# Optimization experiments

Hardware: AMD Instinct MI355X
Metric: run time of the kernel (lower is better)

Reference implementation:

```python
import jax, jax.numpy as jnp
import numpy as np
from jax import lax

INIT_STRIDE = 10.0
COARSE_STRIDE = 4.0
DOWN_SAMPLE = 4.0
NUM_POINT = 128
N_INST = 2000


def setup_inputs() -> dict:
    key = jax.random.key(0)
    ks = jax.random.split(key, 12)
    B, C, H, W = 4, 64, 256, 256
    return {
        'cnn_feature': jax.random.normal(ks[0], (B, C, H, W), jnp.float32),
        'wh_pred': jax.random.normal(ks[1], (B, NUM_POINT * 2, H, W), jnp.float32),
        'ct_ind': jax.random.randint(ks[2], (N_INST,), 0, H * W, jnp.int64 if jax.config.jax_enable_x64 else jnp.int32),
        'ct_img_idx': jax.random.randint(ks[3], (N_INST,), 0, B, jnp.int64 if jax.config.jax_enable_x64 else jnp.int32),
        'conv1_w': jax.random.normal(ks[4], (256, 64, 3, 3), jnp.float32) * 0.05,
        'conv1_b': jax.random.normal(ks[5], (256,), jnp.float32) * 0.05,
        'conv2_w': jax.random.normal(ks[6], (64, 256, 1, 1), jnp.float32) * 0.05,
        'conv2_b': jax.random.normal(ks[7], (64,), jnp.float32) * 0.05,
        'w_poly': jax.random.normal(ks[8], (NUM_POINT * 4, (NUM_POINT + 1) * 64), jnp.float32) * 0.02,
        'w_fuse': jax.random.normal(ks[9], (NUM_POINT * 2, NUM_POINT * 4), jnp.float32) * 0.02,
        'b_fuse': jax.random.normal(ks[10], (NUM_POINT * 2,), jnp.float32) * 0.02,
    }


def bilinear_sample(feat, pts, img_idx):
    # feat [B,C,H,W]; pts [N,P,2] pixel coords; img_idx [N]
    # matches torch grid_sample(align_corners=False, padding_mode='zeros')
    # with grid = pts/(WH/2) - 1  =>  sample coord = pts - 0.5
    B, C, H, W = feat.shape
    sx = pts[..., 0] - 0.5
    sy = pts[..., 1] - 0.5
    x0 = jnp.floor(sx).astype(jnp.int32); x1 = x0 + 1
    y0 = jnp.floor(sy).astype(jnp.int32); y1 = y0 + 1
    wx1 = sx - x0; wx0 = 1.0 - wx1
    wy1 = sy - y0; wy0 = 1.0 - wy1
    bidx = img_idx[:, None].astype(jnp.int32)  # [N,1]

    def corner(yc, xc, w):
        valid = (xc >= 0) & (xc < W) & (yc >= 0) & (yc < H)
        g = feat[bidx, :, jnp.clip(yc, 0, H - 1), jnp.clip(xc, 0, W - 1)]  # [N,P,C]
        return g * (w * valid)[..., None]

    out = (corner(y0, x0, wy0 * wx0) + corner(y0, x1, wy0 * wx1)
           + corner(y1, x0, wy1 * wx0) + corner(y1, x1, wy1 * wx1))
    return out  # [N,P,C]


def _forward(cnn_feature, wh_pred, ct_ind, ct_img_idx, conv1_w, conv1_b, conv2_w, conv2_b, w_poly, w_fuse, b_fuse):
    B, Cf, H, W = cnn_feature.shape
    N = ct_ind.shape[0]
    ct_x = jnp.clip(ct_ind % W, 0, W - 1)
    ct_y = jnp.clip(ct_ind // W, 0, H - 1)
    # gather polygon offsets at center locations: [N, 2*P] -> [N, P, 2]
    ct_offset = wh_pred[ct_img_idx, :, ct_y, ct_x].reshape(N, NUM_POINT, 2)
    ct = jnp.stack([ct_x, ct_y], axis=1).astype(jnp.float32)  # [N,2]
    init_polys = ct_offset * INIT_STRIDE + ct[:, None, :]  # [N,P,2]

    # Refine.trans_feature: conv3x3(64->256)+ReLU -> conv1x1(256->64)
    dn = ('NCHW', 'OIHW', 'NCHW')
    f = lax.conv_general_dilated(cnn_feature, conv1_w, (1, 1), 'SAME', dimension_numbers=dn) + conv1_b[None, :, None, None]
    f = jax.nn.relu(f)
    f = lax.conv_general_dilated(f, conv2_w, (1, 1), 'VALID', dimension_numbers=dn) + conv2_b[None, :, None, None]

    points = jnp.concatenate([ct[:, None, :], init_polys], axis=1)  # [N,P+1,2]
    fp = bilinear_sample(f, points, ct_img_idx)  # [N,P+1,64]
    fp = fp.transpose(0, 2, 1).reshape(N, -1)  # [N, 64*(P+1)] (C-major like torch)

    off = fp @ w_poly.T            # trans_poly (no bias)
    off = off @ w_fuse.T + b_fuse  # trans_fuse
    off = off.reshape(N, NUM_POINT, 2)
    coarse_polys = off * COARSE_STRIDE + lax.stop_gradient(init_polys)
    # stacked outputs: poly_init*down, poly_coarse*down -> [2,N,P,2]
    return jnp.stack([init_polys * DOWN_SAMPLE, coarse_polys * DOWN_SAMPLE])


def reference(cnn_feature, wh_pred, ct_ind, ct_img_idx, conv1_w, conv1_b, conv2_w, conv2_b, w_poly, w_fuse, b_fuse):
    return _forward(cnn_feature, wh_pred, ct_ind, ct_img_idx, conv1_w, conv1_b, conv2_w, conv2_b, w_poly, w_fuse, b_fuse)
```

## Files before the change

kernel.cpp:

```cpp
#include <hip/hip_runtime.h>

typedef unsigned short ushort_t;
typedef __bf16 bf16x8 __attribute__((ext_vector_type(8)));
typedef float f32x4 __attribute__((ext_vector_type(4)));

__device__ __forceinline__ ushort_t f2b(float f) {
  union { float f; unsigned u; } v; v.f = f;
  unsigned r = v.u + 0x7FFFu + ((v.u >> 16) & 1u);
  return (ushort_t)(r >> 16);
}
__device__ __forceinline__ float b2f(ushort_t u) {
  union { unsigned u; float f; } v; v.u = ((unsigned)u) << 16;
  return v.f;
}
__device__ __forceinline__ f32x4 MFMA(bf16x8 a, bf16x8 b, f32x4 c) {
  return __builtin_amdgcn_mfma_f32_16x16x32_bf16(a, b, c, 0, 0, 0);
}
__device__ __forceinline__ void gload_lds16(const ushort_t* g, ushort_t* l) {
  __builtin_amdgcn_global_load_lds(
      (const __attribute__((address_space(1))) unsigned int*)g,
      (__attribute__((address_space(3))) unsigned int*)l, 16, 0, 0);
}

#define XTW 258

__global__ void zero_border_kernel(ushort_t* __restrict__ xt) {
  int i = blockIdx.x * 256 + threadIdx.x;
  if (i >= 32896) return;
  int px_id = i >> 3, oct = (i & 7) << 3;
  int img = px_id / 1028, r = px_id - img * 1028;
  int row, col;
  if (r < 516) { row = (r < 258) ? 0 : 257; col = (r < 258) ? r : r - 258; }
  else { int rr = r - 516; row = 1 + (rr >> 1); col = (rr & 1) ? 257 : 0; }
  uint4 z = make_uint4(0, 0, 0, 0);
  *(uint4*)(xt + (((size_t)img * XTW + row) * XTW + col) * 64 + oct) = z;
}

__global__ void cast_xt_kernel(const float* __restrict__ x, ushort_t* __restrict__ xt) {
  __shared__ float tile[64][65];
  int blk = blockIdx.x;
  int b = blk >> 10, rest = blk & 1023;
  int y = rest >> 2, xseg = (rest & 3) << 6;
  int p0 = y * 256 + xseg;
  int t = threadIdx.x;
#pragma unroll
  for (int rep = 0; rep < 16; ++rep) {
    int lin = rep * 256 + t;
    int c = lin >> 6, p = lin & 63;
    tile[c][p] = x[((size_t)(b * 64 + c)) * 65536 + p0 + p];
  }
  __syncthreads();
#pragma unroll
  for (int rep = 0; rep < 2; ++rep) {
    int u = rep * 256 + t;
    int p = u >> 3, cc = (u & 7) << 3;
    union { ushort_t s[8]; uint4 v; } pk;
#pragma unroll
    for (int j = 0; j < 8; ++j) pk.s[j] = f2b(tile[cc + j][p]);
    int gx = xseg + p + 1;
    size_t base = (((size_t)b * XTW + (y + 1)) * XTW + gx) * 64;
    *(uint4*)(xt + base + (cc ^ ((gx & 7) << 3))) = pk.v;
  }
}

__global__ void cast_w1t_kernel(const float* __restrict__ w1, ushort_t* __restrict__ w1t) {
  int i = blockIdx.x * 256 + threadIdx.x;
  int tap = i >> 14;
  int rem = i & 16383;
  int nn = rem >> 6, c = rem & 63;
  int cs = c ^ ((nn & 7) << 3);
  w1t[tap * 16384 + nn * 64 + cs] = f2b(w1[(nn * 64 + c) * 9 + tap]);
}

__global__ void cast_f32_bf16_kernel(const float* __restrict__ src, ushort_t* __restrict__ dst, int n) {
  for (int i = blockIdx.x * blockDim.x + threadIdx.x; i < n; i += gridDim.x * blockDim.x)
    dst[i] = f2b(src[i]);
}

__global__ void prep_kernel(const float* __restrict__ wh, const int* __restrict__ ct_ind,
                            const int* __restrict__ ct_b, float* __restrict__ out,
                            float* __restrict__ pts) {
  int n = blockIdx.x, t = threadIdx.x;
  int ci = ct_ind[n];
  int b = ct_b[n];
  int ctx = ci & 255;
  int cty = (ci >> 8) & 255;
  float fx = (float)ctx, fy = (float)cty;
  size_t base = ((size_t)b * 256 + 2 * t) * 65536 + (size_t)cty * 256 + ctx;
  float ox = wh[base];
  float oy = wh[base + 65536];
  float ix = ox * 10.f + fx, iy = oy * 10.f + fy;
  out[(n * 128 + t) * 2]     = ix * 4.f;
  out[(n * 128 + t) * 2 + 1] = iy * 4.f;
  float* pn = pts + (size_t)n * 258;
  if (t == 0) { pn[0] = fx; pn[1] = fy; }
  pn[2 + t * 2] = ix;
  pn[3 + t * 2] = iy;
}

__global__ __launch_bounds__(512, 1)
void conv_fused_kernel(const ushort_t* __restrict__ xt, const ushort_t* __restrict__ w1t,
                       const float* __restrict__ b1, const float* __restrict__ w2,
                       const float* __restrict__ b2, ushort_t* __restrict__ f2) {
  __shared__ __align__(16) char smem[163840];
  ushort_t* strip = (ushort_t*)smem;
  ushort_t* Bb0   = (ushort_t*)(smem + 69632);
  ushort_t* Bb1   = (ushort_t*)(smem + 102400);
  ushort_t* F1    = (ushort_t*)smem;
  ushort_t* W2l   = (ushort_t*)(smem + 131072);
  ushort_t* T     = (ushort_t*)smem;

  int rawblk = blockIdx.x;
  int blk = ((rawblk & 7) << 7) + (rawblk >> 3);
  int b = blk >> 8;
  int rest = blk & 255;
  int y2 = (rest >> 1) << 1;
  int x0 = (rest & 1) << 7;
  int tid = threadIdx.x;
  int wid = tid >> 6, lane = tid & 63;
  int l15 = lane & 15, lg = lane >> 4;
  int wm = (wid >> 1) << 6;
  int wn = (wid & 1) << 7;

#pragma unroll
  for (int j = 0; j < 4; ++j) {
    int q = (wid << 2) + j;
    gload_lds16(w1t + q * 512 + lane * 8, Bb0 + q * 512);
  }
#pragma unroll
  for (int j = 0; j < 4; ++j) {
    int q = (wid << 2) + j;
    gload_lds16(w1t + 16384 + q * 512 + lane * 8, Bb1 + q * 512);
  }
  for (int c = wid; c < 68; c += 8) {
    int ry = c / 17, ck = c - ry * 17;
    const ushort_t* g = xt + (((size_t)b * XTW + (y2 + ry)) * XTW + x0 + ck * 8) * 64 + lane * 8;
    gload_lds16(g, strip + (ry * 136 + ck * 8) * 64);
  }
  asm volatile("s_waitcnt vmcnt(0) lgkmcnt(0)" ::: "memory");
  asm volatile("s_barrier" ::: "memory");

  f32x4 acc[4][8] = {};

#pragma unroll
  for (int tap = 0; tap < 9; ++tap) {
    const int dy = tap / 3 - 1, dx = tap % 3 - 1;
    ushort_t* Bcur = (tap & 1) ? Bb1 : Bb0;
    if (tap < 8) {
      ushort_t* Bnxt = (tap & 1) ? Bb0 : Bb1;
      const ushort_t* gb = w1t + (tap + 1) * 16384;
#pragma unroll
      for (int j = 0; j < 4; ++j) {
        int q = (wid << 2) + j;
        gload_lds16(gb + q * 512 + lane * 8, Bnxt + q * 512);
      }
    }
    const int sr  = (wm >> 7) + dy + 1;
    const int spb = (wm & 127) + dx + 1;
#pragma unroll
    for (int kk = 0; kk < 2; ++kk) {
      int c0 = (kk << 5) + (lg << 3);
      bf16x8 a[4];
#pragma unroll
      for (int m = 0; m < 4; ++m) {
        int sp = spb + m * 16 + l15;
        a[m] = *(const bf16x8*)(strip + ((sr * 136 + sp) << 6) + (c0 ^ ((sp & 7) << 3)));
      }
#pragma unroll
      for (int nf = 0; nf < 8; ++nf) {
        int br = wn + nf * 16 + l15;
        bf16x8 bb = *(const bf16x8*)(Bcur + (br << 6) + (c0 ^ ((br & 7) << 3)));
#pragma unroll
        for (int m = 0; m < 4; ++m)
          acc[m][nf] = MFMA(a[m], bb, acc[m][nf]);
      }
    }
    if (tap < 8) {
      asm volatile("s_waitcnt vmcnt(0)" ::: "memory");
      asm volatile("s_barrier" ::: "memory");
    }
  }
  __syncthreads();

#pragma unroll
  for (int nf = 0; nf < 8; ++nf) {
    int ch = wn + nf * 16 + l15;
    float bias = b1[ch];
#pragma unroll
    for (int m = 0; m < 4; ++m) {
#pragma unroll
      for (int r = 0; r < 4; ++r) {
        int p = wm + m * 16 + lg * 4 + r;
        F1[(p << 8) + (ch ^ ((p & 7) << 3))] = f2b(fmaxf(acc[m][nf][r] + bias, 0.f));
      }
    }
  }
#pragma unroll
  for (int it = 0; it < 4; ++it) {
    int u = it * 512 + tid;
    int oc = u >> 5, ic = (u & 31) << 3;
    float4 fa = *(const float4*)(w2 + (oc << 8) + ic);
    float4 fb = *(const float4*)(w2 + (oc << 8) + ic + 4);
    union { ushort_t s[8]; uint4 v; } pk;
    pk.s[0] = f2b(fa.x); pk.s[1] = f2b(fa.y); pk.s[2] = f2b(fa.z); pk.s[3] = f2b(fa.w);
    pk.s[4] = f2b(fb.x); pk.s[5] = f2b(fb.y); pk.s[6] = f2b(fb.z); pk.s[7] = f2b(fb.w);
    *(uint4*)(W2l + (oc << 8) + (ic ^ ((oc & 7) << 3))) = pk.v;
  }
  __syncthreads();
  int wpx = wid << 5;
  f32x4 acc2[2][4] = {};
#pragma unroll
  for (int kc = 0; kc < 8; ++kc) {
    int c0 = (kc << 5) + (lg << 3);
    bf16x8 a2[2];
#pragma unroll
    for (int mm = 0; mm < 2; ++mm) {
      int p = wpx + mm * 16 + l15;
      a2[mm] = *(const bf16x8*)(F1 + (p << 8) + (c0 ^ ((p & 7) << 3)));
    }
#pragma unroll
    for (int nf = 0; nf < 4; ++nf) {
      int oc = nf * 16 + l15;
      bf16x8 bw = *(const bf16x8*)(W2l + (oc << 8) + (c0 ^ ((oc & 7) << 3)));
#pragma unroll
      for (int mm = 0; mm < 2; ++mm)
        acc2[mm][nf] = MFMA(a2[mm], bw, acc2[mm][nf]);
    }
  }
  __syncthreads();
#pragma unroll
  for (int mm = 0; mm < 2; ++mm)
#pragma unroll
    for (int nf = 0; nf < 4; ++nf) {
      int oc = nf * 16 + l15;
      float bias = b2[oc];
#pragma unroll
      for (int r = 0; r < 4; ++r) {
        int p = wpx + mm * 16 + lg * 4 + r;
        T[(p << 6) + (oc ^ ((p & 7) << 3))] = f2b(acc2[mm][nf][r] + bias);
      }
    }
  __syncthreads();
  const size_t imgbase = (size_t)b * 65536;
#pragma unroll
  for (int it = 0; it < 4; ++it) {
    int u = it * 512 + tid;
    int p = u >> 3, co = (u & 7) << 3;
    uint4 v = *(const uint4*)(T + (p << 6) + (co ^ ((p & 7) << 3)));
    int gpx = (y2 + (p >> 7)) * 256 + x0 + (p & 127);
    *(uint4*)(f2 + (imgbase + gpx) * 64 + co) = v;
  }
}

__global__ void sample_kernel(const ushort_t* __restrict__ f2, const float* __restrict__ pts,
                              const int* __restrict__ ct_b, ushort_t* __restrict__ fp) {
  int n = blockIdx.x, t = threadIdx.x;
  __shared__ float pl[258];
  __shared__ __align__(16) ushort_t fpl[8256];
  int b = ct_b[n];
  const ushort_t* fb = f2 + (size_t)b * 4194304;
  for (int i = t; i < 258; i += 128) pl[i] = pts[(size_t)n * 258 + i];
  __syncthreads();
  int c4 = t & 15;
  int ps = t >> 4;
  for (int base = 0; base < 136; base += 8) {
    int pt = base + ps;
    bool live = pt < 129;
    int ptc = live ? pt : 0;
    float px = pl[ptc * 2], py = pl[ptc * 2 + 1];
    float sx = px - 0.5f, sy = py - 0.5f;
    float fx0 = floorf(sx), fy0 = floorf(sy);
    int x0 = (int)fx0, y0 = (int)fy0;
    float wx1 = sx - fx0, wy1 = sy - fy0;
    float wx0 = 1.f - wx1, wy0 = 1.f - wy1;
    float a0 = 0.f, a1 = 0.f, a2 = 0.f, a3 = 0.f;
#pragma unroll
    for (int cy = 0; cy < 2; ++cy) {
#pragma unroll
      for (int cx = 0; cx < 2; ++cx) {
        int yc = y0 + cy, xc = x0 + cx;
        float w = (cy ? wy1 : wy0) * (cx ? wx1 : wx0);
        bool valid = (xc >= 0) && (xc < 256) && (yc >= 0) && (yc < 256);
        int ycc = min(max(yc, 0), 255), xcc = min(max(xc, 0), 255);
        uint2 v = *(const uint2*)(fb + ((size_t)(ycc * 256 + xcc)) * 64 + (c4 << 2));
        float ww = valid ? w : 0.f;
        a0 += b2f((ushort_t)(v.x & 0xFFFF)) * ww;
        a1 += b2f((ushort_t)(v.x >> 16)) * ww;
        a2 += b2f((ushort_t)(v.y & 0xFFFF)) * ww;
        a3 += b2f((ushort_t)(v.y >> 16)) * ww;
      }
    }
    if (live) {
      int ch = c4 << 2;
      fpl[(ch + 0) * 129 + pt] = f2b(a0);
      fpl[(ch + 1) * 129 + pt] = f2b(a1);
      fpl[(ch + 2) * 129 + pt] = f2b(a2);
      fpl[(ch + 3) * 129 + pt] = f2b(a3);
    }
  }
  __syncthreads();
  uint4* fo = (uint4*)(fp + (size_t)n * 8256);
  const uint4* fi = (const uint4*)fpl;
  for (int i = t; i < 1032; i += 128) fo[i] = fi[i];
}

__global__ __launch_bounds__(256)
void gemm_splitk_kernel(const ushort_t* __restrict__ A, const ushort_t* __restrict__ B,
                        float* __restrict__ partials) {
  __shared__ ushort_t Alds[64][72];
  __shared__ ushort_t Blds[64][72];
  int spatial = blockIdx.x;
  int kc = blockIdx.y;
  int xcd = spatial & 7, j = spatial >> 3;
  int m_t = (xcd << 2) + (j >> 3);
  int n_t = j & 7;
  int m0 = m_t << 6, n0 = n_t << 6;
  int ks0 = (129 * kc) >> 3, ks1 = (129 * (kc + 1)) >> 3;

  int tid = threadIdx.x;
  int wid = tid >> 6, lane = tid & 63;
  int l15 = lane & 15, lg = lane >> 4;
  int wm = (wid >> 1) * 32, wn = (wid & 1) * 32;
  f32x4 acc[2][2] = {};
  for (int ks = ks0; ks < ks1; ++ks) {
    __syncthreads();
#pragma unroll
    for (int it = 0; it < 2; ++it) {
      int u = it * 256 + tid;
      int r = u >> 3, cc = (u & 7) << 3;
      int ar = m0 + r; if (ar > 1999) ar = 1999;
      *(uint4*)(&Alds[r][cc]) = *(const uint4*)(A + (size_t)ar * 8256 + ks * 64 + cc);
      *(uint4*)(&Blds[r][cc]) = *(const uint4*)(B + (size_t)(n0 + r) * 8256 + ks * 64 + cc);
    }
    __syncthreads();
#pragma unroll
    for (int kk = 0; kk < 2; ++kk) {
      int c0 = (kk << 5) + (lg << 3);
      bf16x8 a[2], b[2];
      a[0] = *(const bf16x8*)(&Alds[wm + l15][c0]);
      a[1] = *(const bf16x8*)(&Alds[wm + 16 + l15][c0]);
      b[0] = *(const bf16x8*)(&Blds[wn + l15][c0]);
      b[1] = *(const bf16x8*)(&Blds[wn + 16 + l15][c0]);
#pragma unroll
      for (int m = 0; m < 2; ++m)
#pragma unroll
        for (int nf = 0; nf < 2; ++nf)
          acc[m][nf] = MFMA(a[m], b[nf], acc[m][nf]);
    }
  }
  float* pout = partials + (size_t)kc * 1048576;
#pragma unroll
  for (int m = 0; m < 2; ++m)
#pragma unroll
    for (int nf = 0; nf < 2; ++nf)
#pragma unroll
      for (int r = 0; r < 4; ++r) {
        int row = m0 + wm + m * 16 + lg * 4 + r;
        int col = n0 + wn + nf * 16 + l15;
        pout[(size_t)row * 512 + col] = acc[m][nf][r];
      }
}

__global__ void reduce_splitk_kernel(const float* __restrict__ partials,
                                     ushort_t* __restrict__ off1) {
  int i = blockIdx.x * 256 + threadIdx.x;
  size_t idx = (size_t)i * 4;
  float4 s = *(const float4*)(partials + idx);
#pragma unroll
  for (int c = 1; c < 8; ++c) {
    float4 p = *(const float4*)(partials + (size_t)c * 1048576 + idx);
    s.x += p.x; s.y += p.y; s.z += p.z; s.w += p.w;
  }
  union { ushort_t u[4]; uint2 v; } pk;
  pk.u[0] = f2b(s.x); pk.u[1] = f2b(s.y); pk.u[2] = f2b(s.z); pk.u[3] = f2b(s.w);
  *(uint2*)(off1 + idx) = pk.v;
}

__global__ __launch_bounds__(256)
void gemm64_epi_kernel(const ushort_t* __restrict__ A, const ushort_t* __restrict__ B,
                       const float* __restrict__ bias, const float* __restrict__ out0,
                       float* __restrict__ out1, int Mvalid) {
  __shared__ ushort_t Alds[64][72];
  __shared__ ushort_t Blds[64][72];
  const int K = 512;
  int n0 = blockIdx.x * 64, m0 = blockIdx.y * 64;
  int tid = threadIdx.x;
  int wid = tid >> 6, lane = tid & 63;
  int l15 = lane & 15, lg = lane >> 4;
  int wm = (wid >> 1) * 32, wn = (wid & 1) * 32;
  f32x4 acc[2][2] = {};
  for (int ks = 0; ks < K / 64; ++ks) {
    __syncthreads();
#pragma unroll
    for (int it = 0; it < 2; ++it) {
      int u = it * 256 + tid;
      int r = u >> 3, cc = (u & 7) << 3;
      *(uint4*)(&Alds[r][cc]) = *(const uint4*)(A + (size_t)(m0 + r) * K + ks * 64 + cc);
      *(uint4*)(&Blds[r][cc]) = *(const uint4*)(B + (size_t)(n0 + r) * K + ks * 64 + cc);
    }
    __syncthreads();
#pragma unroll
    for (int kk = 0; kk < 2; ++kk) {
      int c0 = (kk << 5) + (lg << 3);
      bf16x8 a[2], b[2];
      a[0] = *(const bf16x8*)(&Alds[wm + l15][c0]);
      a[1] = *(const bf16x8*)(&Alds[wm + 16 + l15][c0]);
      b[0] = *(const bf16x8*)(&Blds[wn + l15][c0]);
      b[1] = *(const bf16x8*)(&Blds[wn + 16 + l15][c0]);
#pragma unroll
      for (int m = 0; m < 2; ++m)
#pragma unroll
        for (int nf = 0; nf < 2; ++nf)
          acc[m][nf] = MFMA(a[m], b[nf], acc[m][nf]);
    }
  }
#pragma unroll
  for (int m = 0; m < 2; ++m)
#pragma unroll
    for (int nf = 0; nf < 2; ++nf)
#pragma unroll
      for (int r = 0; r < 4; ++r) {
        int row = m0 + wm + m * 16 + lg * 4 + r;
        int col = n0 + wn + nf * 16 + l15;
        if (row < Mvalid) {
          float v = acc[m][nf][r] + bias[col];
          out1[(size_t)row * 256 + col] = v * 16.f + out0[(size_t)row * 256 + col];
        }
      }
}

extern "C" void kernel_launch(void* const* d_in, const int* in_sizes, int n_in,
                              void* d_out, int out_size, void* d_ws, size_t ws_size,
                              hipStream_t stream) {
  const float* x    = (const float*)d_in[0];
  const float* wh   = (const float*)d_in[1];
  const int* ct_ind = (const int*)d_in[2];
  const int* ct_b   = (const int*)d_in[3];
  const float* w1   = (const float*)d_in[4];
  const float* b1   = (const float*)d_in[5];
  const float* w2   = (const float*)d_in[6];
  const float* b2   = (const float*)d_in[7];
  const float* wp   = (const float*)d_in[8];
  const float* wf   = (const float*)d_in[9];
  const float* bfu  = (const float*)d_in[10];
  float* out = (float*)d_out;
  char* ws = (char*)d_ws;

  ushort_t* xt    = (ushort_t*)(ws + 0);
  float* partials = (float*)(ws + 0);
  ushort_t* w1t   = (ushort_t*)(ws + 34080768);
  ushort_t* f2    = (ushort_t*)(ws + 34375680);
  ushort_t* wpb   = (ushort_t*)(ws + 67930112);
  ushort_t* wfb   = (ushort_t*)(ws + 76384256);
  ushort_t* fp    = (ushort_t*)(ws + 76646400);
  ushort_t* off1  = (ushort_t*)(ws + 109670400);
  float*    pts   = (float*)(ws + 111767552);

  zero_border_kernel<<<dim3(129), dim3(256), 0, stream>>>(xt);
  cast_xt_kernel<<<dim3(4096), dim3(256), 0, stream>>>(x, xt);
  cast_w1t_kernel<<<dim3(576), dim3(256), 0, stream>>>(w1, w1t);
  cast_f32_bf16_kernel<<<dim3(2064), dim3(256), 0, stream>>>(wp, wpb, 4227072);
  cast_f32_bf16_kernel<<<dim3(64), dim3(256), 0, stream>>>(wf, wfb, 131072);
  prep_kernel<<<dim3(2000), dim3(128), 0, stream>>>(wh, ct_ind, ct_b, out, pts);
  conv_fused_kernel<<<dim3(1024), dim3(512), 0, stream>>>(xt, w1t, b1, w2, b2, f2);
  sample_kernel<<<dim3(2000), dim3(128), 0, stream>>>(f2, pts, ct_b, fp);
  gemm_splitk_kernel<<<dim3(256, 8), dim3(256), 0, stream>>>(fp, wpb, partials);
  reduce_splitk_kernel<<<dim3(1024), dim3(256), 0, stream>>>(partials, off1);
  gemm64_epi_kernel<<<dim3(4, 32), dim3(256), 0, stream>>>(off1, wfb, bfu, out,
                                                           out + 512000, 2000);
}
```

Before: 236.5 us.

## Stream conv weights via registers and enlarge split-K GEMM tiles with swizzled LDS

The conv kernel drops its double-buffered LDS weight tiles. Weights are pre-permuted into an MFMA lane-ready layout and loaded straight into registers, software-pipelined one half-tap ahead, which removes per-tap barriers. The split-K GEMM moves from 64x64 to 128x128 tiles with direct global-to-LDS loads into XOR-swizzled shared memory, so both the sampled features and w_poly are written pre-swizzled. This gives more reuse per loaded byte and fewer blocks, at the cost of higher register pressure. The conv launch bound now asks for 2 blocks per CU, but the kernel still declares 160KB of static shared memory.

```diff
diff --git a/kernel.cpp b/kernel.cpp
--- a/kernel.cpp
+++ b/kernel.cpp
@@ -63,18 +63,28 @@
   }
 }
 
-__global__ void cast_w1t_kernel(const float* __restrict__ w1, ushort_t* __restrict__ w1t) {
+__global__ void cast_w1t_kernel(const float* __restrict__ w1, ushort_t* __restrict__ w1t2) {
   int i = blockIdx.x * 256 + threadIdx.x;
-  int tap = i >> 14;
+  int tap = i / 16384;
   int rem = i & 16383;
   int nn = rem >> 6, c = rem & 63;
-  int cs = c ^ ((nn & 7) << 3);
-  w1t[tap * 16384 + nn * 64 + cs] = f2b(w1[(nn * 64 + c) * 9 + tap]);
+  int g = nn >> 4, l15v = nn & 15;
+  int kk = c >> 5, lg = (c >> 3) & 3, j = c & 7;
+  int lanev = lg * 16 + l15v;
+  w1t2[((tap * 2 + kk) * 16 + g) * 512 + lanev * 8 + j] = f2b(w1[(nn * 64 + c) * 9 + tap]);
 }
 
 __global__ void cast_f32_bf16_kernel(const float* __restrict__ src, ushort_t* __restrict__ dst, int n) {
   for (int i = blockIdx.x * blockDim.x + threadIdx.x; i < n; i += gridDim.x * blockDim.x)
     dst[i] = f2b(src[i]);
+}
+
+__global__ void cast_wp_kernel(const float* __restrict__ src, ushort_t* __restrict__ dst) {
+  for (int i = blockIdx.x * blockDim.x + threadIdx.x; i < 4227072; i += gridDim.x * blockDim.x) {
+    int row = i / 8256;
+    int col = i - row * 8256;
+    dst[row * 8256 + (col ^ ((row & 7) << 3))] = f2b(src[i]);
+  }
 }
 
 __global__ void prep_kernel(const float* __restrict__ wh, const int* __restrict__ ct_ind,
@@ -98,14 +108,12 @@
   pn[3 + t * 2] = iy;
 }
 
-__global__ __launch_bounds__(512, 1)
-void conv_fused_kernel(const ushort_t* __restrict__ xt, const ushort_t* __restrict__ w1t,
+__global__ __launch_bounds__(512, 2)
+void conv_fused_kernel(const ushort_t* __restrict__ xt, const ushort_t* __restrict__ w1t2,
                        const float* __restrict__ b1, const float* __restrict__ w2,
                        const float* __restrict__ b2, ushort_t* __restrict__ f2) {
   __shared__ __align__(16) char smem[163840];
   ushort_t* strip = (ushort_t*)smem;
-  ushort_t* Bb0   = (ushort_t*)(smem + 69632);
-  ushort_t* Bb1   = (ushort_t*)(smem + 102400);
   ushort_t* F1    = (ushort_t*)smem;
   ushort_t* W2l   = (ushort_t*)(smem + 131072);
   ushort_t* T     = (ushort_t*)smem;
@@ -121,64 +129,45 @@
   int l15 = lane & 15, lg = lane >> 4;
   int wm = (wid >> 1) << 6;
   int wn = (wid & 1) << 7;
-
-#pragma unroll
-  for (int j = 0; j < 4; ++j) {
-    int q = (wid << 2) + j;
-    gload_lds16(w1t + q * 512 + lane * 8, Bb0 + q * 512);
-  }
-#pragma unroll
-  for (int j = 0; j < 4; ++j) {
-    int q = (wid << 2) + j;
-    gload_lds16(w1t + 16384 + q * 512 + lane * 8, Bb1 + q * 512);
-  }
+  int g0 = wn >> 4;
+
   for (int c = wid; c < 68; c += 8) {
     int ry = c / 17, ck = c - ry * 17;
     const ushort_t* g = xt + (((size_t)b * XTW + (y2 + ry)) * XTW + x0 + ck * 8) * 64 + lane * 8;
     gload_lds16(g, strip + (ry * 136 + ck * 8) * 64);
   }
-  asm volatile("s_waitcnt vmcnt(0) lgkmcnt(0)" ::: "memory");
-  asm volatile("s_barrier" ::: "memory");
+  bf16x8 Breg[2][8];
+#pragma unroll
+  for (int nf = 0; nf < 8; ++nf)
+    Breg[0][nf] = *(const bf16x8*)(w1t2 + (size_t)(g0 + nf) * 512 + lane * 8);
+  __syncthreads();
 
   f32x4 acc[4][8] = {};
 
 #pragma unroll
-  for (int tap = 0; tap < 9; ++tap) {
+  for (int s = 0; s < 18; ++s) {
+    const int tap = s >> 1, kk = s & 1;
+    const int cur = s & 1;
+    if (s < 17) {
+#pragma unroll
+      for (int nf = 0; nf < 8; ++nf)
+        Breg[cur ^ 1][nf] = *(const bf16x8*)(w1t2 + (size_t)((s + 1) * 16 + g0 + nf) * 512 + lane * 8);
+    }
     const int dy = tap / 3 - 1, dx = tap % 3 - 1;
-    ushort_t* Bcur = (tap & 1) ? Bb1 : Bb0;
-    if (tap < 8) {
-      ushort_t* Bnxt = (tap & 1) ? Bb0 : Bb1;
-      const ushort_t* gb = w1t + (tap + 1) * 16384;
-#pragma unroll
-      for (int j = 0; j < 4; ++j) {
-        int q = (wid << 2) + j;
-        gload_lds16(gb + q * 512 + lane * 8, Bnxt + q * 512);
-      }
-    }
     const int sr  = (wm >> 7) + dy + 1;
     const int spb = (wm & 127) + dx + 1;
-#pragma unroll
-    for (int kk = 0; kk < 2; ++kk) {
-      int c0 = (kk << 5) + (lg << 3);
-      bf16x8 a[4];
-#pragma unroll
-      for (int m = 0; m < 4; ++m) {
-        int sp = spb + m * 16 + l15;
-        a[m] = *(const bf16x8*)(strip + ((sr * 136 + sp) << 6) + (c0 ^ ((sp & 7) << 3)));
-      }
-#pragma unroll
-      for (int nf = 0; nf < 8; ++nf) {
-        int br = wn + nf * 16 + l15;
-        bf16x8 bb = *(const bf16x8*)(Bcur + (br << 6) + (c0 ^ ((br & 7) << 3)));
-#pragma unroll
-        for (int m = 0; m < 4; ++m)
-          acc[m][nf] = MFMA(a[m], bb, acc[m][nf]);
-      }
-    }
-    if (tap < 8) {
-      asm volatile("s_waitcnt vmcnt(0)" ::: "memory");
-      asm volatile("s_barrier" ::: "memory");
-    }
+    const int c0 = (kk << 5) + (lg << 3);
+    bf16x8 a[4];
+#pragma unroll
+    for (int m = 0; m < 4; ++m) {
+      int sp = spb + m * 16 + l15;
+      a[m] = *(const bf16x8*)(strip + ((sr * 136 + sp) << 6) + (c0 ^ ((sp & 7) << 3)));
+    }
+#pragma unroll
+    for (int nf = 0; nf < 8; ++nf)
+#pragma unroll
+      for (int m = 0; m < 4; ++m)
+        acc[m][nf] = MFMA(a[m], Breg[cur][nf], acc[m][nf]);
   }
   __syncthreads();
 
@@ -301,58 +290,67 @@
   __syncthreads();
   uint4* fo = (uint4*)(fp + (size_t)n * 8256);
   const uint4* fi = (const uint4*)fpl;
-  for (int i = t; i < 1032; i += 128) fo[i] = fi[i];
+  int key = n & 7;
+  for (int i = t; i < 1032; i += 128) fo[i ^ key] = fi[i];
 }
 
 __global__ __launch_bounds__(256)
 void gemm_splitk_kernel(const ushort_t* __restrict__ A, const ushort_t* __restrict__ B,
                         float* __restrict__ partials) {
-  __shared__ ushort_t Alds[64][72];
-  __shared__ ushort_t Blds[64][72];
+  __shared__ __align__(16) ushort_t Al[8192];
+  __shared__ __align__(16) ushort_t Bl[8192];
   int spatial = blockIdx.x;
   int kc = blockIdx.y;
-  int xcd = spatial & 7, j = spatial >> 3;
-  int m_t = (xcd << 2) + (j >> 3);
-  int n_t = j & 7;
-  int m0 = m_t << 6, n0 = n_t << 6;
+  int n_t = (spatial & 7) >> 1;
+  int m_t = ((spatial >> 3) << 1) | (spatial & 1);
+  int m0 = m_t << 7, n0 = n_t << 7;
   int ks0 = (129 * kc) >> 3, ks1 = (129 * (kc + 1)) >> 3;
 
   int tid = threadIdx.x;
   int wid = tid >> 6, lane = tid & 63;
   int l15 = lane & 15, lg = lane >> 4;
-  int wm = (wid >> 1) * 32, wn = (wid & 1) * 32;
-  f32x4 acc[2][2] = {};
+  int wm = (wid >> 1) << 6, wn = (wid & 1) << 6;
+  int srow = (lane >> 3);
+  int soct = lane & 7;
+  f32x4 acc[4][4] = {};
   for (int ks = ks0; ks < ks1; ++ks) {
     __syncthreads();
 #pragma unroll
-    for (int it = 0; it < 2; ++it) {
-      int u = it * 256 + tid;
-      int r = u >> 3, cc = (u & 7) << 3;
-      int ar = m0 + r; if (ar > 1999) ar = 1999;
-      *(uint4*)(&Alds[r][cc]) = *(const uint4*)(A + (size_t)ar * 8256 + ks * 64 + cc);
-      *(uint4*)(&Blds[r][cc]) = *(const uint4*)(B + (size_t)(n0 + r) * 8256 + ks * 64 + cc);
+    for (int j = 0; j < 4; ++j) {
+      int q = (wid << 2) + j;
+      int r = (q << 3) + srow;
+      int ar = m0 + r;
+      if (ar >= 2000) ar = 1992 + (ar & 7);
+      gload_lds16(A + (size_t)ar * 8256 + ks * 64 + soct * 8, Al + q * 512);
+      gload_lds16(B + (size_t)(n0 + r) * 8256 + ks * 64 + soct * 8, Bl + q * 512);
     }
     __syncthreads();
 #pragma unroll
     for (int kk = 0; kk < 2; ++kk) {
       int c0 = (kk << 5) + (lg << 3);
-      bf16x8 a[2], b[2];
-      a[0] = *(const bf16x8*)(&Alds[wm + l15][c0]);
-      a[1] = *(const bf16x8*)(&Alds[wm + 16 + l15][c0]);
-      b[0] = *(const bf16x8*)(&Blds[wn + l15][c0]);
-      b[1] = *(const bf16x8*)(&Blds[wn + 16 + l15][c0]);
-#pragma unroll
-      for (int m = 0; m < 2; ++m)
-#pragma unroll
-        for (int nf = 0; nf < 2; ++nf)
+      bf16x8 a[4], b[4];
+#pragma unroll
+      for (int m = 0; m < 4; ++m) {
+        int row = wm + m * 16 + l15;
+        a[m] = *(const bf16x8*)(Al + (row << 6) + (c0 ^ ((row & 7) << 3)));
+      }
+#pragma unroll
+      for (int nf = 0; nf < 4; ++nf) {
+        int row = wn + nf * 16 + l15;
+        b[nf] = *(const bf16x8*)(Bl + (row << 6) + (c0 ^ ((row & 7) << 3)));
+      }
+#pragma unroll
+      for (int m = 0; m < 4; ++m)
+#pragma unroll
+        for (int nf = 0; nf < 4; ++nf)
           acc[m][nf] = MFMA(a[m], b[nf], acc[m][nf]);
     }
   }
   float* pout = partials + (size_t)kc * 1048576;
 #pragma unroll
-  for (int m = 0; m < 2; ++m)
-#pragma unroll
-    for (int nf = 0; nf < 2; ++nf)
+  for (int m = 0; m < 4; ++m)
+#pragma unroll
+    for (int nf = 0; nf < 4; ++nf)
 #pragma unroll
       for (int r = 0; r < 4; ++r) {
         int row = m0 + wm + m * 16 + lg * 4 + r;
@@ -448,7 +446,7 @@
 
   ushort_t* xt    = (ushort_t*)(ws + 0);
   float* partials = (float*)(ws + 0);
-  ushort_t* w1t   = (ushort_t*)(ws + 34080768);
+  ushort_t* w1t2  = (ushort_t*)(ws + 34080768);
   ushort_t* f2    = (ushort_t*)(ws + 34375680);
   ushort_t* wpb   = (ushort_t*)(ws + 67930112);
   ushort_t* wfb   = (ushort_t*)(ws + 76384256);
@@ -458,13 +456,13 @@
 
   zero_border_kernel<<<dim3(129), dim3(256), 0, stream>>>(xt);
   cast_xt_kernel<<<dim3(4096), dim3(256), 0, stream>>>(x, xt);
-  cast_w1t_kernel<<<dim3(576), dim3(256), 0, stream>>>(w1, w1t);
-  cast_f32_bf16_kernel<<<dim3(2064), dim3(256), 0, stream>>>(wp, wpb, 4227072);
+  cast_w1t_kernel<<<dim3(576), dim3(256), 0, stream>>>(w1, w1t2);
+  cast_wp_kernel<<<dim3(2064), dim3(256), 0, stream>>>(wp, wpb);
   cast_f32_bf16_kernel<<<dim3(64), dim3(256), 0, stream>>>(wf, wfb, 131072);
   prep_kernel<<<dim3(2000), dim3(128), 0, stream>>>(wh, ct_ind, ct_b, out, pts);
-  conv_fused_kernel<<<dim3(1024), dim3(512), 0, stream>>>(xt, w1t, b1, w2, b2, f2);
+  conv_fused_kernel<<<dim3(1024), dim3(512), 0, stream>>>(xt, w1t2, b1, w2, b2, f2);
   sample_kernel<<<dim3(2000), dim3(128), 0, stream>>>(f2, pts, ct_b, fp);
-  gemm_splitk_kernel<<<dim3(256, 8), dim3(256), 0, stream>>>(fp, wpb, partials);
+  gemm_splitk_kernel<<<dim3(64, 8), dim3(256), 0, stream>>>(fp, wpb, partials);
   reduce_splitk_kernel<<<dim3(1024), dim3(256), 0, stream>>>(partials, off1);
   gemm64_epi_kernel<<<dim3(4, 32), dim3(256), 0, stream>>>(off1, wfb, bfu, out,
                                                            out + 512000, 2000);
```

After: 224.2 us. 1.06x faster.

## Use 128x128 tiles with direct global-to-LDS loads and pre-swizzled operands in split-K GEMM

Applied to the files above, without the earlier changes.

The split-K GEMM goes from 64x64 to 128x128 output tiles, with each wave computing a 64x64 sub-tile (4x4 MFMA fragments). Operand tiles are loaded with global_load_lds straight into shared memory, replacing register-staged copies. To keep LDS reads bank-conflict free without padding, the producers (sample_kernel for fp, a new cast kernel for w_poly) write data already XOR-swizzled per row. This cuts global reloads per FLOP and load instructions, but quarters the grid to 512 blocks and raises register use per thread.

```diff
diff --git a/kernel.cpp b/kernel.cpp
--- a/kernel.cpp
+++ b/kernel.cpp
@@ -75,6 +75,14 @@
 __global__ void cast_f32_bf16_kernel(const float* __restrict__ src, ushort_t* __restrict__ dst, int n) {
   for (int i = blockIdx.x * blockDim.x + threadIdx.x; i < n; i += gridDim.x * blockDim.x)
     dst[i] = f2b(src[i]);
+}
+
+__global__ void cast_wp_kernel(const float* __restrict__ src, ushort_t* __restrict__ dst) {
+  for (int i = blockIdx.x * blockDim.x + threadIdx.x; i < 4227072; i += gridDim.x * blockDim.x) {
+    int row = i / 8256;
+    int col = i - row * 8256;
+    dst[row * 8256 + (col ^ ((row & 7) << 3))] = f2b(src[i]);
+  }
 }
 
 __global__ void prep_kernel(const float* __restrict__ wh, const int* __restrict__ ct_ind,
@@ -301,58 +309,67 @@
   __syncthreads();
   uint4* fo = (uint4*)(fp + (size_t)n * 8256);
   const uint4* fi = (const uint4*)fpl;
-  for (int i = t; i < 1032; i += 128) fo[i] = fi[i];
+  int key = n & 7;
+  for (int i = t; i < 1032; i += 128) fo[i ^ key] = fi[i];
 }
 
 __global__ __launch_bounds__(256)
 void gemm_splitk_kernel(const ushort_t* __restrict__ A, const ushort_t* __restrict__ B,
                         float* __restrict__ partials) {
-  __shared__ ushort_t Alds[64][72];
-  __shared__ ushort_t Blds[64][72];
+  __shared__ __align__(16) ushort_t Al[8192];
+  __shared__ __align__(16) ushort_t Bl[8192];
   int spatial = blockIdx.x;
   int kc = blockIdx.y;
-  int xcd = spatial & 7, j = spatial >> 3;
-  int m_t = (xcd << 2) + (j >> 3);
-  int n_t = j & 7;
-  int m0 = m_t << 6, n0 = n_t << 6;
+  int n_t = (spatial & 7) >> 1;
+  int m_t = ((spatial >> 3) << 1) | (spatial & 1);
+  int m0 = m_t << 7, n0 = n_t << 7;
   int ks0 = (129 * kc) >> 3, ks1 = (129 * (kc + 1)) >> 3;
 
   int tid = threadIdx.x;
   int wid = tid >> 6, lane = tid & 63;
   int l15 = lane & 15, lg = lane >> 4;
-  int wm = (wid >> 1) * 32, wn = (wid & 1) * 32;
-  f32x4 acc[2][2] = {};
+  int wm = (wid >> 1) << 6, wn = (wid & 1) << 6;
+  int srow = (lane >> 3);
+  int soct = lane & 7;
+  f32x4 acc[4][4] = {};
   for (int ks = ks0; ks < ks1; ++ks) {
     __syncthreads();
 #pragma unroll
-    for (int it = 0; it < 2; ++it) {
-      int u = it * 256 + tid;
-      int r = u >> 3, cc = (u & 7) << 3;
-      int ar = m0 + r; if (ar > 1999) ar = 1999;
-      *(uint4*)(&Alds[r][cc]) = *(const uint4*)(A + (size_t)ar * 8256 + ks * 64 + cc);
-      *(uint4*)(&Blds[r][cc]) = *(const uint4*)(B + (size_t)(n0 + r) * 8256 + ks * 64 + cc);
+    for (int j = 0; j < 4; ++j) {
+      int q = (wid << 2) + j;
+      int r = (q << 3) + srow;
+      int ar = m0 + r;
+      if (ar >= 2000) ar = 1992 + (ar & 7);
+      gload_lds16(A + (size_t)ar * 8256 + ks * 64 + soct * 8, Al + q * 512);
+      gload_lds16(B + (size_t)(n0 + r) * 8256 + ks * 64 + soct * 8, Bl + q * 512);
     }
     __syncthreads();
 #pragma unroll
     for (int kk = 0; kk < 2; ++kk) {
       int c0 = (kk << 5) + (lg << 3);
-      bf16x8 a[2], b[2];
-      a[0] = *(const bf16x8*)(&Alds[wm + l15][c0]);
-      a[1] = *(const bf16x8*)(&Alds[wm + 16 + l15][c0]);
-      b[0] = *(const bf16x8*)(&Blds[wn + l15][c0]);
-      b[1] = *(const bf16x8*)(&Blds[wn + 16 + l15][c0]);
-#pragma unroll
-      for (int m = 0; m < 2; ++m)
-#pragma unroll
-        for (int nf = 0; nf < 2; ++nf)
+      bf16x8 a[4], b[4];
+#pragma unroll
+      for (int m = 0; m < 4; ++m) {
+        int row = wm + m * 16 + l15;
+        a[m] = *(const bf16x8*)(Al + (row << 6) + (c0 ^ ((row & 7) << 3)));
+      }
+#pragma unroll
+      for (int nf = 0; nf < 4; ++nf) {
+        int row = wn + nf * 16 + l15;
+        b[nf] = *(const bf16x8*)(Bl + (row << 6) + (c0 ^ ((row & 7) << 3)));
+      }
+#pragma unroll
+      for (int m = 0; m < 4; ++m)
+#pragma unroll
+        for (int nf = 0; nf < 4; ++nf)
           acc[m][nf] = MFMA(a[m], b[nf], acc[m][nf]);
     }
   }
   float* pout = partials + (size_t)kc * 1048576;
 #pragma unroll
-  for (int m = 0; m < 2; ++m)
-#pragma unroll
-    for (int nf = 0; nf < 2; ++nf)
+  for (int m = 0; m < 4; ++m)
+#pragma unroll
+    for (int nf = 0; nf < 4; ++nf)
 #pragma unroll
       for (int r = 0; r < 4; ++r) {
         int row = m0 + wm + m * 16 + lg * 4 + r;
@@ -459,12 +476,12 @@
   zero_border_kernel<<<dim3(129), dim3(256), 0, stream>>>(xt);
   cast_xt_kernel<<<dim3(4096), dim3(256), 0, stream>>>(x, xt);
   cast_w1t_kernel<<<dim3(576), dim3(256), 0, stream>>>(w1, w1t);
-  cast_f32_bf16_kernel<<<dim3(2064), dim3(256), 0, stream>>>(wp, wpb, 4227072);
+  cast_wp_kernel<<<dim3(2064), dim3(256), 0, stream>>>(wp, wpb);
   cast_f32_bf16_kernel<<<dim3(64), dim3(256), 0, stream>>>(wf, wfb, 131072);
   prep_kernel<<<dim3(2000), dim3(128), 0, stream>>>(wh, ct_ind, ct_b, out, pts);
   conv_fused_kernel<<<dim3(1024), dim3(512), 0, stream>>>(xt, w1t, b1, w2, b2, f2);
   sample_kernel<<<dim3(2000), dim3(128), 0, stream>>>(f2, pts, ct_b, fp);
-  gemm_splitk_kernel<<<dim3(256, 8), dim3(256), 0, stream>>>(fp, wpb, partials);
+  gemm_splitk_kernel<<<dim3(64, 8), dim3(256), 0, stream>>>(fp, wpb, partials);
   reduce_splitk_kernel<<<dim3(1024), dim3(256), 0, stream>>>(partials, off1);
   gemm64_epi_kernel<<<dim3(4, 32), dim3(256), 0, stream>>>(off1, wfb, bfu, out,
                                                            out + 512000, 2000);
```

Measured after the change: 221.4 us. -6.4%, faster.
